# Optimization experiments

Hardware: AMD Instinct MI355X
Metric: run time of the kernel (lower is better)

Reference implementation:

```python
import jax, jax.numpy as jnp
import numpy as np

M, E, H, V = 8, 512, 1024, 4096
BI = 4096  # rows per ensemble member
LN_EPS = 1e-5


def setup_inputs() -> dict:
    key = jax.random.key(0)
    ks = jax.random.split(key, 5)
    s1 = 1.0 / np.sqrt(E)
    s2 = 1.0 / np.sqrt(H)
    return {
        "x": jax.random.normal(ks[0], (M * BI, E), dtype=jnp.float32),
        "W1": jax.random.uniform(ks[1], (M, E, H), dtype=jnp.float32, minval=-s1, maxval=s1),
        "b1": jax.random.uniform(ks[2], (M, H), dtype=jnp.float32, minval=-s1, maxval=s1),
        "ln_w": jnp.ones((M, H), dtype=jnp.float32),
        "ln_b": jnp.zeros((M, H), dtype=jnp.float32),
        "W2": jax.random.uniform(ks[3], (M, H, V), dtype=jnp.float32, minval=-s2, maxval=s2),
        "b2": jax.random.uniform(ks[4], (M, V), dtype=jnp.float32, minval=-s2, maxval=s2),
    }


def reference(x, W1, b1, ln_w, ln_b, W2, b2):
    # x: [(m*bi), E] -> [m, bi, E]  (each member processes its batch slice)
    xm = x.reshape(M, BI, E)
    # Linear 1 (batched grouped GEMM over members)
    h = jnp.einsum("mbe,meh->mbh", xm, W1) + b1[:, None, :]
    # LayerNorm over last dim
    mu = jnp.mean(h, axis=-1, keepdims=True)
    var = jnp.mean(jnp.square(h - mu), axis=-1, keepdims=True)
    h = (h - mu) * jax.lax.rsqrt(var + LN_EPS)
    h = h * ln_w[:, None, :] + ln_b[:, None, :]
    # SiLU
    h = h * jax.nn.sigmoid(h)
    # Linear 2
    out = jnp.einsum("mbh,mhv->mbv", h, W2) + b2[:, None, :]
    # [m, bi, V] -> [(m*bi), V]
    return out.reshape(M * BI, V)
```

## Files before the change

### kernel.cpp

```cpp
#include <hip/hip_runtime.h>

#define M_MEMBERS 8
#define E_DIM 512
#define H_DIM 1024
#define V_DIM 4096
#define BI_DIM 4096

typedef __bf16 bf16x8 __attribute__((ext_vector_type(8)));
typedef float f32x4 __attribute__((ext_vector_type(4)));

__device__ __forceinline__ unsigned short f2b(float f) {
    unsigned u = __builtin_bit_cast(unsigned, f);
    u += 0x7fffu + ((u >> 16) & 1u);
    return (unsigned short)(u >> 16);
}
__device__ __forceinline__ float b2f(unsigned short s) {
    return __builtin_bit_cast(float, (unsigned)s << 16);
}

typedef unsigned int __attribute__((address_space(1)))* gas_ptr;
typedef unsigned int __attribute__((address_space(3)))* las_ptr;

__device__ __forceinline__ void async16(const void* g, void* l) {
    __builtin_amdgcn_global_load_lds((gas_ptr)(unsigned long long)g,
                                     (las_ptr)(unsigned)(unsigned long long)l,
                                     16, 0, 0);
}

__global__ __launch_bounds__(256) void cvt_bf16(const float* __restrict__ in,
                                                unsigned short* __restrict__ out, long n) {
    long i = ((long)blockIdx.x * blockDim.x + threadIdx.x) * 4;
    if (i + 3 < n) {
        float4 v = *(const float4*)(in + i);
        ushort4 o;
        o.x = f2b(v.x); o.y = f2b(v.y); o.z = f2b(v.z); o.w = f2b(v.w);
        *(ushort4*)(out + i) = o;
    }
}

__global__ __launch_bounds__(256) void cvt_t(const float* __restrict__ in,
                                             unsigned short* __restrict__ out,
                                             int R, int C) {
    __shared__ unsigned short tile[32][34];
    const long mb = blockIdx.z;
    const float* inp = in + mb * (long)R * C;
    unsigned short* outp = out + mb * (long)R * C;
    const int c0 = blockIdx.x * 32, r0 = blockIdx.y * 32;
    const int tx = threadIdx.x, ty = threadIdx.y;
#pragma unroll
    for (int i = 0; i < 32; i += 8)
        tile[ty + i][tx] = f2b(inp[(long)(r0 + ty + i) * C + c0 + tx]);
    __syncthreads();
#pragma unroll
    for (int i = 0; i < 32; i += 8)
        outp[(long)(c0 + ty + i) * R + r0 + tx] = tile[tx][ty + i];
}

template <bool OUT_BF16>
__global__ __launch_bounds__(256, 2) void gemm_bt(
    const unsigned short* __restrict__ A,
    const unsigned short* __restrict__ Bt,
    const float* __restrict__ bias,
    void* __restrict__ Cout,
    int N, int K,
    long sA, long sB, long sBias, long sC)
{
    __shared__ __align__(16) unsigned short ldsA[128 * 32];
    __shared__ __align__(16) unsigned short ldsB[128 * 32];

    const int tid  = threadIdx.x;
    const int wave = tid >> 6;
    const int lane = tid & 63;
    const int wr   = wave >> 1;
    const int wc   = wave & 1;
    const long mb  = blockIdx.z;

    const unsigned short* Ag = A  + mb * sA + (long)blockIdx.x * 128 * K;
    const unsigned short* Bg = Bt + mb * sB + (long)blockIdx.y * 128 * K;

    const int srow = wave * 16 + (lane >> 2);
    const int scol = (lane & 3) * 8;
    const unsigned short* agp = Ag + (long)srow * K + scol;
    const unsigned short* bgp = Bg + (long)srow * K + scol;
    unsigned short* la_w = &ldsA[wave * 16 * 32];
    unsigned short* lb_w = &ldsB[wave * 16 * 32];

    f32x4 acc[4][4] = {};

    const int frow = lane & 15;
    const int qk   = (lane >> 4) * 8;

    for (int k0 = 0; k0 < K; k0 += 32) {
        async16(agp + k0,            la_w);
        async16(agp + k0 + 64 * K,   la_w + 64 * 32);
        async16(bgp + k0,            lb_w);
        async16(bgp + k0 + 64 * K,   lb_w + 64 * 32);
        __syncthreads();

        bf16x8 af[4], bfr[4];
#pragma unroll
        for (int t = 0; t < 4; t++) {
            af[t]  = *(const bf16x8*)&ldsA[(wr * 64 + t * 16 + frow) * 32 + qk];
            bfr[t] = *(const bf16x8*)&ldsB[(wc * 64 + t * 16 + frow) * 32 + qk];
        }
#pragma unroll
        for (int i = 0; i < 4; i++)
#pragma unroll
            for (int j = 0; j < 4; j++)
                acc[i][j] = __builtin_amdgcn_mfma_f32_16x16x32_bf16(af[i], bfr[j], acc[i][j], 0, 0, 0);
        __syncthreads();
    }

    const int row0 = blockIdx.x * 128 + wr * 64 + (lane >> 4) * 4;
    const int col0 = blockIdx.y * 128 + wc * 64 + (lane & 15);
    const float* bp = bias + mb * sBias;
#pragma unroll
    for (int tj = 0; tj < 4; tj++) {
        const int c = col0 + tj * 16;
        const float bv = bp[c];
#pragma unroll
        for (int ti = 0; ti < 4; ti++) {
            const int r = row0 + ti * 16;
#pragma unroll
            for (int e = 0; e < 4; e++) {
                float v = acc[ti][tj][e] + bv;
                if (OUT_BF16)
                    ((unsigned short*)Cout)[mb * sC + (long)(r + e) * N + c] = f2b(v);
                else
                    ((float*)Cout)[mb * sC + (long)(r + e) * N + c] = v;
            }
        }
    }
}

__global__ __launch_bounds__(256) void ln_silu(unsigned short* __restrict__ h,
                                               const float* __restrict__ lnw,
                                               const float* __restrict__ lnb) {
    const long row = blockIdx.x;
    const int m = (int)(row >> 12);
    unsigned short* hp = h + row * H_DIM;
    const int tid = threadIdx.x;

    ushort4 raw = *(const ushort4*)(hp + tid * 4);
    float v0 = b2f(raw.x), v1 = b2f(raw.y), v2 = b2f(raw.z), v3 = b2f(raw.w);
    float s  = v0 + v1 + v2 + v3;
    float s2 = v0 * v0 + v1 * v1 + v2 * v2 + v3 * v3;
#pragma unroll
    for (int off = 32; off > 0; off >>= 1) {
        s  += __shfl_down(s,  off, 64);
        s2 += __shfl_down(s2, off, 64);
    }
    __shared__ float wsum[4], wsq[4];
    const int wave = tid >> 6, lane = tid & 63;
    if (lane == 0) { wsum[wave] = s; wsq[wave] = s2; }
    __syncthreads();
    const float S  = wsum[0] + wsum[1] + wsum[2] + wsum[3];
    const float S2 = wsq[0] + wsq[1] + wsq[2] + wsq[3];
    const float mu  = S * (1.0f / H_DIM);
    const float var = S2 * (1.0f / H_DIM) - mu * mu;
    const float rs  = rsqrtf(var + 1e-5f);

    const float* wp = lnw + (long)m * H_DIM + tid * 4;
    const float* bp = lnb + (long)m * H_DIM + tid * 4;
    float t0 = (v0 - mu) * rs * wp[0] + bp[0];
    float t1 = (v1 - mu) * rs * wp[1] + bp[1];
    float t2 = (v2 - mu) * rs * wp[2] + bp[2];
    float t3 = (v3 - mu) * rs * wp[3] + bp[3];
    ushort4 o;
    o.x = f2b(t0 / (1.0f + __expf(-t0)));
    o.y = f2b(t1 / (1.0f + __expf(-t1)));
    o.z = f2b(t2 / (1.0f + __expf(-t2)));
    o.w = f2b(t3 / (1.0f + __expf(-t3)));
    *(ushort4*)(hp + tid * 4) = o;
}

extern "C" void kernel_launch(void* const* d_in, const int* in_sizes, int n_in,
                              void* d_out, int out_size, void* d_ws, size_t ws_size,
                              hipStream_t stream) {
    (void)in_sizes; (void)n_in; (void)out_size; (void)ws_size;
    const float* x   = (const float*)d_in[0];
    const float* W1  = (const float*)d_in[1];
    const float* b1  = (const float*)d_in[2];
    const float* lnw = (const float*)d_in[3];
    const float* lnb = (const float*)d_in[4];
    const float* W2  = (const float*)d_in[5];
    const float* b2  = (const float*)d_in[6];
    float* out = (float*)d_out;

    const size_t nX  = (size_t)M_MEMBERS * BI_DIM * E_DIM;
    const size_t nW1 = (size_t)M_MEMBERS * E_DIM * H_DIM;
    const size_t nW2 = (size_t)M_MEMBERS * H_DIM * V_DIM;
    unsigned short* xb  = (unsigned short*)d_ws;
    unsigned short* w1t = xb  + nX;
    unsigned short* w2t = w1t + nW1;
    unsigned short* hb  = w2t + nW2;

    cvt_bf16<<<(unsigned)(nX / 1024), 256, 0, stream>>>(x, xb, (long)nX);
    cvt_t<<<dim3(H_DIM / 32, E_DIM / 32, M_MEMBERS), dim3(32, 8), 0, stream>>>(W1, w1t, E_DIM, H_DIM);
    cvt_t<<<dim3(V_DIM / 32, H_DIM / 32, M_MEMBERS), dim3(32, 8), 0, stream>>>(W2, w2t, H_DIM, V_DIM);

    gemm_bt<true><<<dim3(BI_DIM / 128, H_DIM / 128, M_MEMBERS), 256, 0, stream>>>(
        xb, w1t, b1, hb, H_DIM, E_DIM,
        (long)BI_DIM * E_DIM, (long)H_DIM * E_DIM, (long)H_DIM, (long)BI_DIM * H_DIM);

    ln_silu<<<dim3(M_MEMBERS * BI_DIM), 256, 0, stream>>>(hb, lnw, lnb);

    gemm_bt<false><<<dim3(BI_DIM / 128, V_DIM / 128, M_MEMBERS), 256, 0, stream>>>(
        hb, w2t, b2, out, V_DIM, H_DIM,
        (long)BI_DIM * H_DIM, (long)V_DIM * H_DIM, (long)V_DIM, (long)BI_DIM * V_DIM);
}
```

Baseline: 1.077 ms.

## Replace GEMM with 256x256 double-buffered, swizzled-LDS, 8-wave pipelined kernel

Replaces the 128x128 single-buffer GEMM with a 256x256 tile per 512-thread block, using K-steps of 64, double-buffered LDS and an XOR swizzle to avoid bank conflicts. Global-to-LDS async loads for the next K tile are interleaved with four MFMA quadrant phases, gated by explicit vmcnt waits and barriers, and MFMA runs at raised wave priority. The aim is higher arithmetic intensity per byte loaded and overlap of memory traffic with matrix math. In exchange it uses 64KB of LDS and more accumulator registers per block, and the hand-written wait and barrier schedule is fragile.

```diff
diff --git a/kernel.cpp b/kernel.cpp
--- a/kernel.cpp
+++ b/kernel.cpp
@@ -56,8 +56,59 @@
         outp[(long)(c0 + ty + i) * R + r0 + tx] = tile[tx][ty + i];
 }
 
+#define VMWAIT(n) asm volatile("s_waitcnt vmcnt(" #n ")" ::: "memory")
+#define BAR() __builtin_amdgcn_s_barrier()
+
+#define STAGE(mat, half, base, k0, p)                                              \
+    do {                                                                           \
+        const int _r = tid >> 3;                                                   \
+        const int _c = (tid & 7) ^ (_r & 7);                                       \
+        const unsigned short* _g =                                                 \
+            (base) + (long)((half) * 128 + _r) * K + (k0) + _c * 8;                \
+        unsigned short* _lb = &lds[p][mat][half][wave * 512];                      \
+        async16(_g, _lb);                                                          \
+        async16(_g + 64 * (long)K, _lb + 4096);                                    \
+    } while (0)
+
+#define LDA(p, qm)                                                                 \
+    _Pragma("unroll")                                                              \
+    for (int _m = 0; _m < 4; _m++) {                                               \
+        _Pragma("unroll")                                                          \
+        for (int _kk = 0; _kk < 2; _kk++) {                                        \
+            const int _r = wr * 64 + _m * 16 + frow;                               \
+            af[_m][_kk] = *(const bf16x8*)                                         \
+                &lds[p][0][qm][_r * 64 + (((_kk * 4 + kq) ^ (_r & 7)) * 8)];       \
+        }                                                                          \
+    }
+
+#define LDB(p, qn)                                                                 \
+    _Pragma("unroll")                                                              \
+    for (int _n = 0; _n < 2; _n++) {                                               \
+        _Pragma("unroll")                                                          \
+        for (int _kk = 0; _kk < 2; _kk++) {                                        \
+            const int _r = wc * 32 + _n * 16 + frow;                               \
+            bfr[_n][_kk] = *(const bf16x8*)                                        \
+                &lds[p][1][qn][_r * 64 + (((_kk * 4 + kq) ^ (_r & 7)) * 8)];       \
+        }                                                                          \
+    }
+
+#define MFMA16(qm, qn)                                                             \
+    __builtin_amdgcn_s_setprio(1);                                                 \
+    _Pragma("unroll")                                                              \
+    for (int _m = 0; _m < 4; _m++) {                                               \
+        _Pragma("unroll")                                                          \
+        for (int _n = 0; _n < 2; _n++) {                                           \
+            _Pragma("unroll")                                                      \
+            for (int _kk = 0; _kk < 2; _kk++) {                                    \
+                acc[qm][qn][_m][_n] = __builtin_amdgcn_mfma_f32_16x16x32_bf16(     \
+                    af[_m][_kk], bfr[_n][_kk], acc[qm][qn][_m][_n], 0, 0, 0);      \
+            }                                                                      \
+        }                                                                          \
+    }                                                                              \
+    __builtin_amdgcn_s_setprio(0);
+
 template <bool OUT_BF16>
-__global__ __launch_bounds__(256, 2) void gemm_bt(
+__global__ __launch_bounds__(512, 2) void gemm256(
     const unsigned short* __restrict__ A,
     const unsigned short* __restrict__ Bt,
     const float* __restrict__ bias,
@@ -65,69 +116,97 @@
     int N, int K,
     long sA, long sB, long sBias, long sC)
 {
-    __shared__ __align__(16) unsigned short ldsA[128 * 32];
-    __shared__ __align__(16) unsigned short ldsB[128 * 32];
+    __shared__ __align__(16) unsigned short lds[2][2][2][128 * 64];
 
     const int tid  = threadIdx.x;
     const int wave = tid >> 6;
     const int lane = tid & 63;
-    const int wr   = wave >> 1;
-    const int wc   = wave & 1;
+    const int wr   = wave >> 2;
+    const int wc   = wave & 3;
+    const int frow = lane & 15;
+    const int kq   = lane >> 4;
     const long mb  = blockIdx.z;
 
-    const unsigned short* Ag = A  + mb * sA + (long)blockIdx.x * 128 * K;
-    const unsigned short* Bg = Bt + mb * sB + (long)blockIdx.y * 128 * K;
-
-    const int srow = wave * 16 + (lane >> 2);
-    const int scol = (lane & 3) * 8;
-    const unsigned short* agp = Ag + (long)srow * K + scol;
-    const unsigned short* bgp = Bg + (long)srow * K + scol;
-    unsigned short* la_w = &ldsA[wave * 16 * 32];
-    unsigned short* lb_w = &ldsB[wave * 16 * 32];
-
-    f32x4 acc[4][4] = {};
-
-    const int frow = lane & 15;
-    const int qk   = (lane >> 4) * 8;
-
-    for (int k0 = 0; k0 < K; k0 += 32) {
-        async16(agp + k0,            la_w);
-        async16(agp + k0 + 64 * K,   la_w + 64 * 32);
-        async16(bgp + k0,            lb_w);
-        async16(bgp + k0 + 64 * K,   lb_w + 64 * 32);
-        __syncthreads();
-
-        bf16x8 af[4], bfr[4];
-#pragma unroll
-        for (int t = 0; t < 4; t++) {
-            af[t]  = *(const bf16x8*)&ldsA[(wr * 64 + t * 16 + frow) * 32 + qk];
-            bfr[t] = *(const bf16x8*)&ldsB[(wc * 64 + t * 16 + frow) * 32 + qk];
-        }
-#pragma unroll
-        for (int i = 0; i < 4; i++)
-#pragma unroll
-            for (int j = 0; j < 4; j++)
-                acc[i][j] = __builtin_amdgcn_mfma_f32_16x16x32_bf16(af[i], bfr[j], acc[i][j], 0, 0, 0);
-        __syncthreads();
-    }
-
-    const int row0 = blockIdx.x * 128 + wr * 64 + (lane >> 4) * 4;
-    const int col0 = blockIdx.y * 128 + wc * 64 + (lane & 15);
+    const unsigned short* Ag = A  + mb * sA + (long)blockIdx.x * 256 * K;
+    const unsigned short* Bg = Bt + mb * sB + (long)blockIdx.y * 256 * K;
+
+    f32x4  acc[2][2][4][2] = {};
+    bf16x8 af[4][2];
+    bf16x8 bfr[2][2];
+
+    STAGE(0, 0, Ag, 0, 0);
+    STAGE(1, 0, Bg, 0, 0);
+    STAGE(1, 1, Bg, 0, 0);
+    STAGE(0, 1, Ag, 0, 0);
+    VMWAIT(4);
+    BAR();
+
+    const int NT = K >> 6;
+    for (int t = 0; t < NT - 1; ++t) {
+        const int p  = t & 1;
+        const int pn = p ^ 1;
+        const int k1 = (t + 1) << 6;
+        LDA(p, 0); LDB(p, 0);
+        STAGE(0, 0, Ag, k1, pn);
+        BAR();
+        MFMA16(0, 0);
+        VMWAIT(4);
+        BAR();
+        LDB(p, 1);
+        STAGE(1, 0, Bg, k1, pn);
+        BAR();
+        MFMA16(0, 1);
+        VMWAIT(4);
+        BAR();
+        LDA(p, 1);
+        STAGE(1, 1, Bg, k1, pn);
+        BAR();
+        MFMA16(1, 1);
+        BAR();
+        LDB(p, 0);
+        STAGE(0, 1, Ag, k1, pn);
+        BAR();
+        MFMA16(1, 0);
+        VMWAIT(4);
+        BAR();
+    }
+    {
+        const int p = (NT - 1) & 1;
+        LDA(p, 0); LDB(p, 0);
+        MFMA16(0, 0);
+        VMWAIT(2); BAR();
+        LDB(p, 1);
+        MFMA16(0, 1);
+        VMWAIT(0); BAR();
+        LDA(p, 1);
+        MFMA16(1, 1);
+        LDB(p, 0);
+        MFMA16(1, 0);
+    }
+
     const float* bp = bias + mb * sBias;
-#pragma unroll
-    for (int tj = 0; tj < 4; tj++) {
-        const int c = col0 + tj * 16;
-        const float bv = bp[c];
-#pragma unroll
-        for (int ti = 0; ti < 4; ti++) {
-            const int r = row0 + ti * 16;
-#pragma unroll
-            for (int e = 0; e < 4; e++) {
-                float v = acc[ti][tj][e] + bv;
-                if (OUT_BF16)
-                    ((unsigned short*)Cout)[mb * sC + (long)(r + e) * N + c] = f2b(v);
-                else
-                    ((float*)Cout)[mb * sC + (long)(r + e) * N + c] = v;
+    const int r_base = blockIdx.x * 256 + wr * 64 + (lane >> 4) * 4;
+    const int c_base = blockIdx.y * 256 + wc * 32 + (lane & 15);
+#pragma unroll
+    for (int qm = 0; qm < 2; qm++) {
+#pragma unroll
+        for (int qn = 0; qn < 2; qn++) {
+#pragma unroll
+            for (int m = 0; m < 4; m++) {
+#pragma unroll
+                for (int n = 0; n < 2; n++) {
+                    const int r = r_base + qm * 128 + m * 16;
+                    const int c = c_base + qn * 128 + n * 16;
+                    const float bv = bp[c];
+#pragma unroll
+                    for (int e = 0; e < 4; e++) {
+                        float v = acc[qm][qn][m][n][e] + bv;
+                        if (OUT_BF16)
+                            ((unsigned short*)Cout)[mb * sC + (long)(r + e) * N + c] = f2b(v);
+                        else
+                            ((float*)Cout)[mb * sC + (long)(r + e) * N + c] = v;
+                    }
+                }
             }
         }
     }
@@ -199,13 +278,13 @@
     cvt_t<<<dim3(H_DIM / 32, E_DIM / 32, M_MEMBERS), dim3(32, 8), 0, stream>>>(W1, w1t, E_DIM, H_DIM);
     cvt_t<<<dim3(V_DIM / 32, H_DIM / 32, M_MEMBERS), dim3(32, 8), 0, stream>>>(W2, w2t, H_DIM, V_DIM);
 
-    gemm_bt<true><<<dim3(BI_DIM / 128, H_DIM / 128, M_MEMBERS), 256, 0, stream>>>(
+    gemm256<true><<<dim3(BI_DIM / 256, H_DIM / 256, M_MEMBERS), 512, 0, stream>>>(
         xb, w1t, b1, hb, H_DIM, E_DIM,
         (long)BI_DIM * E_DIM, (long)H_DIM * E_DIM, (long)H_DIM, (long)BI_DIM * H_DIM);
 
     ln_silu<<<dim3(M_MEMBERS * BI_DIM), 256, 0, stream>>>(hb, lnw, lnb);
 
-    gemm_bt<false><<<dim3(BI_DIM / 128, V_DIM / 128, M_MEMBERS), 256, 0, stream>>>(
+    gemm256<false><<<dim3(BI_DIM / 256, V_DIM / 256, M_MEMBERS), 512, 0, stream>>>(
         hb, w2t, b2, out, V_DIM, H_DIM,
         (long)BI_DIM * H_DIM, (long)V_DIM * H_DIM, (long)V_DIM, (long)BI_DIM * V_DIM);
 }
```

After: 973.8 us. -9.6%, faster.
